# Performance work log

Measured on AMD Instinct MI355X. Metric: run time of the kernel, lower is better.

## Reference

```python
import jax, jax.numpy as jnp
import numpy as np

N_NODES = 100000
N_EDGES = 1600000
HIDDEN = 128
N_LAYERS = 4
EPS = 0.0  # GINConv default eps, train_eps=False


def setup_inputs() -> dict:
    key = jax.random.key(0)
    ks = jax.random.split(key, 6)
    scale = 1.0 / np.sqrt(HIDDEN)
    return {
        "x": jax.random.normal(ks[0], (N_NODES, HIDDEN), dtype=jnp.float32),
        "edge_index": jax.random.randint(ks[1], (2, N_EDGES), 0, N_NODES, dtype=jnp.int64),
        "W1": jax.random.normal(ks[2], (N_LAYERS, HIDDEN, HIDDEN), dtype=jnp.float32) * scale,
        "b1": jnp.zeros((N_LAYERS, HIDDEN), dtype=jnp.float32),
        "W2": jax.random.normal(ks[3], (N_LAYERS, HIDDEN, HIDDEN), dtype=jnp.float32) * scale,
        "b2": jnp.zeros((N_LAYERS, HIDDEN), dtype=jnp.float32),
    }


def reference(x, edge_index, W1, b1, W2, b2):
    src = edge_index[0]  # message sources (x_j)
    dst = edge_index[1]  # aggregation targets
    n = x.shape[0]
    for l in range(N_LAYERS):
        x_in = x
        # scatter-add aggregation: sum_{j in N(i)} x_j
        agg = jax.ops.segment_sum(x[src], dst, num_segments=n)
        out = agg + (1.0 + EPS) * x
        # GIN MLP: Linear -> ReLU -> Linear
        h = jax.nn.relu(out @ W1[l] + b1[l]) @ W2[l] + b2[l]
        # outer loop: relu, dropout (identity in eval), residual
        x = x_in + jax.nn.relu(h)
    return x
```

## Files before the change

### kernel.cpp

```cpp
#include <hip/hip_runtime.h>

typedef unsigned short u16;
typedef unsigned int u32;

constexpr int NN = 100000;
constexpr int NE = 1600000;
constexpr int H = 128;

constexpr int NB = 196;
constexpr int BCAP = 10240;
constexpr int PB_E = 4096;
constexpr int PB_BLOCKS = (NE + PB_E - 1) / PB_E;

typedef __bf16 bf16x8 __attribute__((ext_vector_type(8)));
typedef float f32x16 __attribute__((ext_vector_type(16)));

__device__ __forceinline__ u16 f2bf(float f) {
    union { float f; u32 u; } cv; cv.f = f;
    u32 r = (cv.u + 0x7fffu + ((cv.u >> 16) & 1u)) >> 16;
    return (u16)r;
}
__device__ __forceinline__ float bflo(u32 u) {
    union { u32 u; float f; } cv; cv.u = u << 16; return cv.f;
}
__device__ __forceinline__ float bfhi(u32 u) {
    union { u32 u; float f; } cv; cv.u = u & 0xffff0000u; return cv.f;
}

__global__ void detect_kernel(const int* __restrict__ e, int* __restrict__ flag,
                              int* __restrict__ gcursor) {
    __shared__ int anynz;
    if (threadIdx.x == 0) anynz = 0;
    __syncthreads();
    int local = 0;
    for (int i = threadIdx.x; i < 4096; i += 256)
        if (e[2 * i + 1] != 0) local = 1;
    if (local) atomicOr(&anynz, 1);
    __syncthreads();
    if (threadIdx.x == 0) flag[0] = anynz ? 1 : 2;
    if (threadIdx.x < NB) gcursor[threadIdx.x] = 0;
}

__global__ __launch_bounds__(256) void part_kernel(const int* __restrict__ e,
                                                   const int* __restrict__ flag,
                                                   int* __restrict__ gcursor,
                                                   u32* __restrict__ ebuf) {
    __shared__ int lcnt[NB];
    __shared__ int gbaseL[NB];
    const int t = threadIdx.x;
    if (t < NB) lcnt[t] = 0;
    __syncthreads();
    const int st = flag[0];
    const int base = blockIdx.x * PB_E;
    u32 pk[16]; int bk[16]; int rk[16];
#pragma unroll
    for (int j = 0; j < 16; ++j) {
        int i = base + j * 256 + t;
        bk[j] = -1;
        if (i < NE) {
            int s = e[st * i];
            int d = e[st * (NE + i)];
            int b = d >> 9;
            pk[j] = (u32)s | ((u32)(d & 511) << 17);
            bk[j] = b;
            rk[j] = atomicAdd(&lcnt[b], 1);
        }
    }
    __syncthreads();
    if (t < NB) gbaseL[t] = atomicAdd(&gcursor[t], lcnt[t]);
    __syncthreads();
#pragma unroll
    for (int j = 0; j < 16; ++j)
        if (bk[j] >= 0)
            ebuf[bk[j] * BCAP + gbaseL[bk[j]] + rk[j]] = pk[j];
}

__global__ __launch_bounds__(256) void bscan_kernel(const int* __restrict__ gcursor,
                                                    int* __restrict__ bbase,
                                                    int* __restrict__ offs) {
    __shared__ int s[256];
    int t = threadIdx.x;
    int v = (t < NB) ? gcursor[t] : 0;
    s[t] = v;
    __syncthreads();
    for (int off = 1; off < 256; off <<= 1) {
        int u = (t >= off) ? s[t - off] : 0;
        __syncthreads();
        s[t] += u;
        __syncthreads();
    }
    if (t < NB) bbase[t] = s[t] - v;
    if (t == 0) offs[NN] = NE;
}

__global__ __launch_bounds__(256) void bfill_kernel(const u32* __restrict__ ebuf,
                                                    const int* __restrict__ gcursor,
                                                    const int* __restrict__ bbase,
                                                    int* __restrict__ offs,
                                                    int* __restrict__ colv) {
    __shared__ int ncnt[512];
    __shared__ int cur[512];
    __shared__ int ps[256];
    const int b = blockIdx.x, t = threadIdx.x;
    const int En = gcursor[b];
    const int bb = bbase[b];
    ncnt[t] = 0; ncnt[t + 256] = 0;
    __syncthreads();
    const u32* eb = ebuf + b * BCAP;
    for (int i = t; i < En; i += 256)
        atomicAdd(&ncnt[eb[i] >> 17], 1);
    __syncthreads();
    int s2 = ncnt[2 * t] + ncnt[2 * t + 1];
    ps[t] = s2;
    __syncthreads();
    for (int off = 1; off < 256; off <<= 1) {
        int u = (t >= off) ? ps[t - off] : 0;
        __syncthreads();
        ps[t] += u;
        __syncthreads();
    }
    int e0 = ps[t] - s2;
    cur[2 * t] = e0;
    cur[2 * t + 1] = e0 + ncnt[2 * t];
    __syncthreads();
    const int n0 = b * 512;
    for (int i = t; i < 512; i += 256)
        if (n0 + i < NN) offs[n0 + i] = bb + cur[i];
    __syncthreads();
    for (int i = t; i < En; i += 256) {
        u32 p = eb[i];
        int pos = atomicAdd(&cur[p >> 17], 1);
        colv[bb + pos] = (int)((p & 0x1FFFFu) | (((p >> 17) & 31u) << 27));
    }
}

__global__ void wtconv_kernel(const float* __restrict__ W1,
                              const float* __restrict__ W2,
                              u16* __restrict__ wt) {
    int t = blockIdx.x * 256 + threadIdx.x;
    int w = t >> 14;
    int r = t & 16383;
    int k = r >> 7, n = r & 127;
    int l = w >> 1, s = w & 1;
    const float* src = (s == 0 ? W1 : W2) + l * 16384;
    wt[w * 16384 + n * 128 + k] = f2bf(src[k * 128 + n]);
}

__global__ void xinit_kernel(const float* __restrict__ xin,
                             float* __restrict__ x, u16* __restrict__ xb) {
    int i = blockIdx.x * 256 + threadIdx.x;
    float4 v = ((const float4*)xin)[i];
    ((float4*)x)[i] = v;
    uint2 p;
    p.x = (u32)f2bf(v.x) | ((u32)f2bf(v.y) << 16);
    p.y = (u32)f2bf(v.z) | ((u32)f2bf(v.w) << 16);
    ((uint2*)xb)[i] = p;
}

__global__ __launch_bounds__(256) void mlp_kernel(const u16* __restrict__ xbin,
                                                  const int* __restrict__ colv,
                                                  const int* __restrict__ offs,
                                                  const u16* __restrict__ wt1,
                                                  const u16* __restrict__ wt2,
                                                  const float* __restrict__ b1,
                                                  const float* __restrict__ b2,
                                                  float* __restrict__ x,
                                                  u16* __restrict__ xbout) {
    __shared__ u16 lds[32 * 128];
    const int tid = threadIdx.x;
    const int wave = tid >> 6, lane = tid & 63;
    const int ml = lane & 31, g = lane >> 5;
    const int row0 = blockIdx.x * 32;

#pragma unroll
    for (int i = 0; i < 2; ++i) {
        int ch = tid + 256 * i;
        int r = ch >> 4, c = ch & 15;
        int gr = row0 + r;
        int4 v = *(const int4*)(xbin + gr * H + c * 8);
        *(int4*)(&lds[r * H + ((c ^ (r & 15)) << 3)]) = v;
    }
    __syncthreads();

    {
        const int node0 = row0 + wave * 8;
        const int jb = __builtin_amdgcn_readfirstlane(offs[node0]);
        const int je = __builtin_amdgcn_readfirstlane(offs[node0 + 8]);
        int cur = wave * 8;
        float a0 = 0.f, a1 = 0.f;
        if (jb < je) {
            u32 ce[16];
#pragma unroll
            for (int q = 0; q < 16; ++q) {
                int idx = jb + q;
                idx = idx < je ? idx : je - 1;
                ce[q] = (u32)__builtin_amdgcn_readfirstlane(colv[idx]);
            }
            for (int j = jb; j < je; j += 16) {
                u32 uu[16];
#pragma unroll
                for (int q = 0; q < 16; ++q)
                    uu[q] = *(const u32*)(xbin + (ce[q] & 0x1FFFFu) * H + lane * 2);
                u32 cn[16];
#pragma unroll
                for (int q = 0; q < 16; ++q) {
                    int idx = j + 16 + q;
                    idx = idx < je ? idx : je - 1;
                    cn[q] = (u32)__builtin_amdgcn_readfirstlane(colv[idx]);
                }
#pragma unroll
                for (int q = 0; q < 16; ++q) {
                    if (j + q < je) {
                        int rloc = (int)(ce[q] >> 27);
                        if (rloc != cur) {
                            u16* p = &lds[cur * H + (((lane >> 2) ^ (cur & 15)) << 3) + ((lane & 3) << 1)];
                            u32 old = *(u32*)p;
                            *(u32*)p = (u32)f2bf(bflo(old) + a0) | ((u32)f2bf(bfhi(old) + a1) << 16);
                            a0 = 0.f; a1 = 0.f; cur = rloc;
                        }
                        a0 += bflo(uu[q]); a1 += bfhi(uu[q]);
                    }
                }
#pragma unroll
                for (int q = 0; q < 16; ++q) ce[q] = cn[q];
            }
        }
        u16* p = &lds[cur * H + (((lane >> 2) ^ (cur & 15)) << 3) + ((lane & 3) << 1)];
        u32 old = *(u32*)p;
        *(u32*)p = (u32)f2bf(bflo(old) + a0) | ((u32)f2bf(bfhi(old) + a1) << 16);
    }

    bf16x8 bfrag[8];
#pragma unroll
    for (int ks = 0; ks < 8; ++ks)
        bfrag[ks] = *(const bf16x8*)(wt1 + (wave * 32 + ml) * H + ks * 16 + g * 8);

    const float bias1 = b1[wave * 32 + ml];
    const float bias2 = b2[wave * 32 + ml];

    __syncthreads();

    f32x16 acc;
#pragma unroll
    for (int i = 0; i < 16; ++i) acc[i] = 0.f;

#pragma unroll
    for (int ks = 0; ks < 8; ++ks) {
        int chunk = (2 * ks + g) ^ (ml & 15);
        bf16x8 afrag = *(const bf16x8*)(&lds[ml * H + (chunk << 3)]);
        acc = __builtin_amdgcn_mfma_f32_32x32x16_bf16(afrag, bfrag[ks], acc, 0, 0, 0);
    }

    __syncthreads();

#pragma unroll
    for (int reg = 0; reg < 16; ++reg) {
        int rm = (reg & 3) + ((reg >> 2) << 3) + 4 * g;
        int cn = wave * 32 + ml;
        float v = acc[reg] + bias1;
        v = v > 0.f ? v : 0.f;
        lds[rm * H + ((((cn >> 3) ^ (rm & 15))) << 3) + (cn & 7)] = f2bf(v);
    }

#pragma unroll
    for (int ks = 0; ks < 8; ++ks)
        bfrag[ks] = *(const bf16x8*)(wt2 + (wave * 32 + ml) * H + ks * 16 + g * 8);

#pragma unroll
    for (int i = 0; i < 16; ++i) acc[i] = 0.f;

    __syncthreads();

#pragma unroll
    for (int ks = 0; ks < 8; ++ks) {
        int chunk = (2 * ks + g) ^ (ml & 15);
        bf16x8 afrag = *(const bf16x8*)(&lds[ml * H + (chunk << 3)]);
        acc = __builtin_amdgcn_mfma_f32_32x32x16_bf16(afrag, bfrag[ks], acc, 0, 0, 0);
    }

    __syncthreads();

#pragma unroll
    for (int reg = 0; reg < 16; ++reg) {
        int rm = (reg & 3) + ((reg >> 2) << 3) + 4 * g;
        int cn = wave * 32 + ml;
        float v = acc[reg] + bias2;
        v = v > 0.f ? v : 0.f;
        lds[rm * H + ((((cn >> 3) ^ (rm & 15))) << 3) + (cn & 7)] = f2bf(v);
    }

    __syncthreads();

#pragma unroll
    for (int i = 0; i < 2; ++i) {
        int ch = tid + 256 * i;
        int r = ch >> 4, c = ch & 15;
        int gr = row0 + r;
        int4 hv = *(const int4*)(&lds[r * H + ((c ^ (r & 15)) << 3)]);
        float4 x0 = *(const float4*)(x + gr * H + c * 8);
        float4 x1 = *(const float4*)(x + gr * H + c * 8 + 4);
        x0.x += bflo((u32)hv.x); x0.y += bfhi((u32)hv.x);
        x0.z += bflo((u32)hv.y); x0.w += bfhi((u32)hv.y);
        x1.x += bflo((u32)hv.z); x1.y += bfhi((u32)hv.z);
        x1.z += bflo((u32)hv.w); x1.w += bfhi((u32)hv.w);
        *(float4*)(x + gr * H + c * 8) = x0;
        *(float4*)(x + gr * H + c * 8 + 4) = x1;
        int4 xo;
        xo.x = (int)((u32)f2bf(x0.x) | ((u32)f2bf(x0.y) << 16));
        xo.y = (int)((u32)f2bf(x0.z) | ((u32)f2bf(x0.w) << 16));
        xo.z = (int)((u32)f2bf(x1.x) | ((u32)f2bf(x1.y) << 16));
        xo.w = (int)((u32)f2bf(x1.z) | ((u32)f2bf(x1.w) << 16));
        *(int4*)(xbout + gr * H + c * 8) = xo;
    }
}

extern "C" void kernel_launch(void* const* d_in, const int* in_sizes, int n_in,
                              void* d_out, int out_size, void* d_ws, size_t ws_size,
                              hipStream_t stream) {
    const float* x_in = (const float*)d_in[0];
    const int* edges = (const int*)d_in[1];
    const float* W1 = (const float*)d_in[2];
    const float* b1 = (const float*)d_in[3];
    const float* W2 = (const float*)d_in[4];
    const float* b2 = (const float*)d_in[5];
    float* x = (float*)d_out;

    char* ws = (char*)d_ws;
    int* flag = (int*)ws;
    int* gcursor = (int*)(ws + 512);
    int* bbase = (int*)(ws + 2048);
    int* offs = (int*)(ws + 4096);
    int* colv = (int*)(ws + 406528);
    u16* wt = (u16*)(ws + 6809600);
    u16* xb0 = (u16*)(ws + 7072768);
    u16* xb1 = (u16*)(ws + 32672768);
    u32* ebuf = (u32*)xb1;

    detect_kernel<<<1, 256, 0, stream>>>(edges, flag, gcursor);
    part_kernel<<<PB_BLOCKS, 256, 0, stream>>>(edges, flag, gcursor, ebuf);
    bscan_kernel<<<1, 256, 0, stream>>>(gcursor, bbase, offs);
    bfill_kernel<<<NB, 256, 0, stream>>>(ebuf, gcursor, bbase, offs, colv);
    wtconv_kernel<<<131072 / 256, 256, 0, stream>>>(W1, W2, wt);
    xinit_kernel<<<(NN * H / 4) / 256, 256, 0, stream>>>(x_in, x, xb0);

    for (int l = 0; l < 4; ++l) {
        u16* xin = (l & 1) ? xb1 : xb0;
        u16* xout = (l & 1) ? xb0 : xb1;
        mlp_kernel<<<NN / 32, 256, 0, stream>>>(
            xin, colv, offs,
            wt + (l * 2) * 16384, wt + (l * 2 + 1) * 16384,
            b1 + l * 128, b2 + l * 128, x, xout);
    }
}
```

Measured before the change: 490.1 us.

## Coalesce partition scatter via LDS staging and merge setup kernels

The partition kernel now sorts each block's edges by bucket in shared memory, using a prefix scan over local counts, before writing them to the global bucket buffers. Consecutive threads therefore store consecutive addresses instead of scattering. The separate detect kernel is removed: every partition block redundantly re-checks the int64 layout itself, and the cursor reset becomes a memset. The weight-conversion and x-init kernels are merged into one launch, and the MLP weight and bias loads are hoisted ahead of aggregation so their latency can overlap. These changes cut launches and scatter traffic, at the cost of extra shared memory and scan synchronisation per block.

```diff
diff --git a/kernel.cpp b/kernel.cpp
--- a/kernel.cpp
+++ b/kernel.cpp
@@ -2,6 +2,7 @@
 
 typedef unsigned short u16;
 typedef unsigned int u32;
+typedef unsigned char u8;
 
 constexpr int NN = 100000;
 constexpr int NE = 1600000;
@@ -27,31 +28,27 @@
     union { u32 u; float f; } cv; cv.u = u & 0xffff0000u; return cv.f;
 }
 
-__global__ void detect_kernel(const int* __restrict__ e, int* __restrict__ flag,
-                              int* __restrict__ gcursor) {
-    __shared__ int anynz;
-    if (threadIdx.x == 0) anynz = 0;
-    __syncthreads();
-    int local = 0;
-    for (int i = threadIdx.x; i < 4096; i += 256)
-        if (e[2 * i + 1] != 0) local = 1;
-    if (local) atomicOr(&anynz, 1);
-    __syncthreads();
-    if (threadIdx.x == 0) flag[0] = anynz ? 1 : 2;
-    if (threadIdx.x < NB) gcursor[threadIdx.x] = 0;
-}
-
 __global__ __launch_bounds__(256) void part_kernel(const int* __restrict__ e,
-                                                   const int* __restrict__ flag,
                                                    int* __restrict__ gcursor,
                                                    u32* __restrict__ ebuf) {
-    __shared__ int lcnt[NB];
+    __shared__ int lcnt[256];
+    __shared__ int ps[256];
+    __shared__ int ex[256];
     __shared__ int gbaseL[NB];
+    __shared__ int anynz;
+    __shared__ u32 sbuf[PB_E];
+    __shared__ u8 sbk[PB_E];
     const int t = threadIdx.x;
-    if (t < NB) lcnt[t] = 0;
-    __syncthreads();
-    const int st = flag[0];
+    if (t == 0) anynz = 0;
+    lcnt[t] = 0;
+    __syncthreads();
+    int loc = 0;
+    for (int i = t; i < 4096; i += 256) loc |= e[2 * i + 1];
+    if (loc) atomicOr(&anynz, 1);
+    __syncthreads();
+    const int st = anynz ? 1 : 2;
     const int base = blockIdx.x * PB_E;
+    const int nval = (NE - base < PB_E) ? (NE - base) : PB_E;
     u32 pk[16]; int bk[16]; int rk[16];
 #pragma unroll
     for (int j = 0; j < 16; ++j) {
@@ -67,12 +64,30 @@
         }
     }
     __syncthreads();
-    if (t < NB) gbaseL[t] = atomicAdd(&gcursor[t], lcnt[t]);
+    int v = lcnt[t];
+    ps[t] = v;
+    __syncthreads();
+    for (int off = 1; off < 256; off <<= 1) {
+        int u = (t >= off) ? ps[t - off] : 0;
+        __syncthreads();
+        ps[t] += u;
+        __syncthreads();
+    }
+    ex[t] = ps[t] - v;
+    if (t < NB && v > 0) gbaseL[t] = atomicAdd(&gcursor[t], v);
     __syncthreads();
 #pragma unroll
     for (int j = 0; j < 16; ++j)
-        if (bk[j] >= 0)
-            ebuf[bk[j] * BCAP + gbaseL[bk[j]] + rk[j]] = pk[j];
+        if (bk[j] >= 0) {
+            int p = ex[bk[j]] + rk[j];
+            sbuf[p] = pk[j];
+            sbk[p] = (u8)bk[j];
+        }
+    __syncthreads();
+    for (int i = t; i < nval; i += 256) {
+        int b = sbk[i];
+        ebuf[b * BCAP + gbaseL[b] + (i - ex[b])] = sbuf[i];
+    }
 }
 
 __global__ __launch_bounds__(256) void bscan_kernel(const int* __restrict__ gcursor,
@@ -134,27 +149,29 @@
     }
 }
 
-__global__ void wtconv_kernel(const float* __restrict__ W1,
-                              const float* __restrict__ W2,
-                              u16* __restrict__ wt) {
-    int t = blockIdx.x * 256 + threadIdx.x;
-    int w = t >> 14;
-    int r = t & 16383;
-    int k = r >> 7, n = r & 127;
-    int l = w >> 1, s = w & 1;
-    const float* src = (s == 0 ? W1 : W2) + l * 16384;
-    wt[w * 16384 + n * 128 + k] = f2bf(src[k * 128 + n]);
-}
-
-__global__ void xinit_kernel(const float* __restrict__ xin,
-                             float* __restrict__ x, u16* __restrict__ xb) {
-    int i = blockIdx.x * 256 + threadIdx.x;
-    float4 v = ((const float4*)xin)[i];
-    ((float4*)x)[i] = v;
-    uint2 p;
-    p.x = (u32)f2bf(v.x) | ((u32)f2bf(v.y) << 16);
-    p.y = (u32)f2bf(v.z) | ((u32)f2bf(v.w) << 16);
-    ((uint2*)xb)[i] = p;
+__global__ void init_kernel(const float* __restrict__ W1,
+                            const float* __restrict__ W2,
+                            u16* __restrict__ wt,
+                            const float* __restrict__ xin,
+                            float* __restrict__ x, u16* __restrict__ xb) {
+    int b = blockIdx.x;
+    if (b < 512) {
+        int t = b * 256 + threadIdx.x;
+        int w = t >> 14;
+        int r = t & 16383;
+        int k = r >> 7, n = r & 127;
+        int l = w >> 1, s = w & 1;
+        const float* src = (s == 0 ? W1 : W2) + l * 16384;
+        wt[w * 16384 + n * 128 + k] = f2bf(src[k * 128 + n]);
+    } else {
+        int i = (b - 512) * 256 + threadIdx.x;
+        float4 v = ((const float4*)xin)[i];
+        ((float4*)x)[i] = v;
+        uint2 p;
+        p.x = (u32)f2bf(v.x) | ((u32)f2bf(v.y) << 16);
+        p.y = (u32)f2bf(v.z) | ((u32)f2bf(v.w) << 16);
+        ((uint2*)xb)[i] = p;
+    }
 }
 
 __global__ __launch_bounds__(256) void mlp_kernel(const u16* __restrict__ xbin,
@@ -172,6 +189,13 @@
     const int ml = lane & 31, g = lane >> 5;
     const int row0 = blockIdx.x * 32;
 
+    bf16x8 bfrag[8];
+#pragma unroll
+    for (int ks = 0; ks < 8; ++ks)
+        bfrag[ks] = *(const bf16x8*)(wt1 + (wave * 32 + ml) * H + ks * 16 + g * 8);
+    const float bias1 = b1[wave * 32 + ml];
+    const float bias2 = b2[wave * 32 + ml];
+
 #pragma unroll
     for (int i = 0; i < 2; ++i) {
         int ch = tid + 256 * i;
@@ -229,14 +253,6 @@
         u32 old = *(u32*)p;
         *(u32*)p = (u32)f2bf(bflo(old) + a0) | ((u32)f2bf(bfhi(old) + a1) << 16);
     }
-
-    bf16x8 bfrag[8];
-#pragma unroll
-    for (int ks = 0; ks < 8; ++ks)
-        bfrag[ks] = *(const bf16x8*)(wt1 + (wave * 32 + ml) * H + ks * 16 + g * 8);
-
-    const float bias1 = b1[wave * 32 + ml];
-    const float bias2 = b2[wave * 32 + ml];
 
     __syncthreads();
 
@@ -326,7 +342,6 @@
     float* x = (float*)d_out;
 
     char* ws = (char*)d_ws;
-    int* flag = (int*)ws;
     int* gcursor = (int*)(ws + 512);
     int* bbase = (int*)(ws + 2048);
     int* offs = (int*)(ws + 4096);
@@ -336,12 +351,11 @@
     u16* xb1 = (u16*)(ws + 32672768);
     u32* ebuf = (u32*)xb1;
 
-    detect_kernel<<<1, 256, 0, stream>>>(edges, flag, gcursor);
-    part_kernel<<<PB_BLOCKS, 256, 0, stream>>>(edges, flag, gcursor, ebuf);
+    hipMemsetAsync(gcursor, 0, NB * sizeof(int), stream);
+    part_kernel<<<PB_BLOCKS, 256, 0, stream>>>(edges, gcursor, ebuf);
     bscan_kernel<<<1, 256, 0, stream>>>(gcursor, bbase, offs);
     bfill_kernel<<<NB, 256, 0, stream>>>(ebuf, gcursor, bbase, offs, colv);
-    wtconv_kernel<<<131072 / 256, 256, 0, stream>>>(W1, W2, wt);
-    xinit_kernel<<<(NN * H / 4) / 256, 256, 0, stream>>>(x_in, x, xb0);
+    init_kernel<<<512 + (NN * H / 4) / 256, 256, 0, stream>>>(W1, W2, wt, x_in, x, xb0);
 
     for (int l = 0; l < 4; ++l) {
         u16* xin = (l & 1) ? xb1 : xb0;
```

Result: no change. 485.5 us (-0.9%).
